# Kernel optimization log

Hardware: AMD Instinct MI355X
Metric: run time of the kernel (lower is better)

The kernel has to match this reference:

```python
import jax, jax.numpy as jnp
import numpy as np
import math

DIM = 512
BLOCK_NUM = 16
SEQ_LEN = 8192
BLOCK_LEN = SEQ_LEN // BLOCK_NUM  # 512 == DIM -> mask used as-is
BATCH = 4
LN_EPS = 1e-3  # keras LayerNormalization default epsilon


def setup_inputs() -> dict:
    key = jax.random.key(0)
    ks = jax.random.split(key, 5)
    inputs = jax.random.normal(ks[0], (BATCH, BLOCK_NUM, BLOCK_LEN, DIM), dtype=jnp.float32)
    # binary padding-style mask, values in {0,1}
    mask_array = jax.random.randint(ks[1], (BATCH, SEQ_LEN, DIM), 0, 2).astype(jnp.float32)
    scale = 1.0 / math.sqrt(DIM)
    dw1 = jax.random.normal(ks[2], (DIM, DIM), dtype=jnp.float32) * scale
    dw2 = jax.random.normal(ks[3], (DIM, DIM), dtype=jnp.float32) * scale
    dw3 = jax.random.normal(ks[4], (DIM, DIM), dtype=jnp.float32) * scale
    db1 = jnp.zeros((DIM,), dtype=jnp.float32)
    db2 = jnp.zeros((DIM,), dtype=jnp.float32)
    db3 = jnp.zeros((DIM,), dtype=jnp.float32)
    return {"inputs": inputs, "mask_array": mask_array,
            "dw1": dw1, "dw2": dw2, "dw3": dw3,
            "db1": db1, "db2": db2, "db3": db3}


def reference(inputs, mask_array, dw1, dw2, dw3, db1, db2, db3):
    # inputs: [B, block_num, block_len, dim]
    Q = jnp.matmul(inputs, dw1) + db1
    K = jnp.matmul(inputs, dw2) + db2
    V = jnpp_matmul = jnp.matmul(inputs, dw3) + db3
    V = jnp.matmul(inputs, dw3) + db3
    # block-local attention scores: [B, bn, bl, bl]
    scores = jnp.einsum('bnqd,bnkd->bnqk', Q, K) / math.sqrt(DIM)
    # mask: [B, seq_len, dim] -> [B, bn, bl, dim]; block_len == dim so no slice/tile
    m = mask_array.reshape(BATCH, BLOCK_NUM, BLOCK_LEN, DIM)
    scores = scores + (1.0 - m) * jnp.float32(-1e10)
    p = jax.nn.softmax(scores, axis=-1)
    out = jnp.einsum('bnqk,bnkd->bnqd', p, V) + inputs  # residual
    # LayerNorm(axis=-1), fresh keras layer: gamma=1, beta=0, eps=1e-3
    mean = jnp.mean(out, axis=-1, keepdims=True)
    var = jnp.mean(jnp.square(out - mean), axis=-1, keepdims=True)
    return (out - mean) / jnp.sqrt(var + LN_EPS)
```

## Files before the change

kernel.cpp:

```cpp
#include <hip/hip_runtime.h>

#define DIMK 512
#define NBLK 64
#define NTOK 32768

typedef short  short8 __attribute__((ext_vector_type(8)));
typedef float  f32x4  __attribute__((ext_vector_type(4)));
typedef unsigned short u16x8 __attribute__((ext_vector_type(8)));

__device__ __forceinline__ unsigned short f2bf(float f) {
  union { float f; unsigned u; } v; v.f = f;
  unsigned r = (v.u + 0x7FFFu + ((v.u >> 16) & 1u)) >> 16;
  return (unsigned short)r;
}
__device__ __forceinline__ float bf2f(unsigned short h) {
  return __uint_as_float(((unsigned)h) << 16);
}

__device__ __forceinline__ void gload_lds16(const unsigned short* g,
                                            unsigned short* l) {
  __builtin_amdgcn_global_load_lds(
      (const __attribute__((address_space(1))) unsigned int*)(g),
      (__attribute__((address_space(3))) unsigned int*)(l),
      16, 0, 0);
}


__global__ __launch_bounds__(256) void k_wt_prep(
    const float* __restrict__ dw1, const float* __restrict__ dw2,
    const float* __restrict__ dw3, unsigned short* __restrict__ Wt)
{
  __shared__ float t[64][65];
  const int b = blockIdx.x;
  const int w = b >> 6;
  const int tt = b & 63;
  const int kt = (tt >> 3) * 64;
  const int nt = (tt & 7) * 64;
  const float* dw = (w == 0) ? dw1 : (w == 1) ? dw2 : dw3;
  const int tid = threadIdx.x;
  const int rr = tid >> 4;
  const int cc = (tid & 15) << 2;

#pragma unroll
  for (int p = 0; p < 4; ++p) {
    const int r = rr + p * 16;
    const float4 v = *(const float4*)&dw[(size_t)(kt + r) * 512 + nt + cc];
    t[cc + 0][r] = v.x; t[cc + 1][r] = v.y;
    t[cc + 2][r] = v.z; t[cc + 3][r] = v.w;
  }
  __syncthreads();
#pragma unroll
  for (int p = 0; p < 4; ++p) {
    const int r = rr + p * 16;
    const int n = nt + r;
    const int k = kt + cc;
    ushort4 o;
    o.x = f2bf(t[r][cc + 0]); o.y = f2bf(t[r][cc + 1]);
    o.z = f2bf(t[r][cc + 2]); o.w = f2bf(t[r][cc + 3]);
    *(ushort4*)&Wt[(size_t)w * 262144 + (size_t)(k >> 5) * 16384 +
                   (size_t)n * 32 + (k & 31)] = o;
  }
}

__global__ __launch_bounds__(256) void k_xconv(
    const float* __restrict__ X, unsigned short* __restrict__ Xb)
{
  const size_t gid = (size_t)blockIdx.x * 256 + threadIdx.x;
  const size_t i = gid * 8;
  const int tok = (int)(i >> 9);
  const int col = (int)(i & 511);
  const float4 a = *(const float4*)(X + i);
  const float4 b = *(const float4*)(X + i + 4);
  u16x8 o;
  o[0] = f2bf(a.x); o[1] = f2bf(a.y); o[2] = f2bf(a.z); o[3] = f2bf(a.w);
  o[4] = f2bf(b.x); o[5] = f2bf(b.y); o[6] = f2bf(b.z); o[7] = f2bf(b.w);
  *(u16x8*)(Xb + ((size_t)(tok >> 7) * 16 + (col >> 5)) * 4096 +
            (tok & 127) * 32 + (col & 31)) = o;
}

__global__ __launch_bounds__(256) void k_bitpack(
    const float* __restrict__ mask, unsigned char* __restrict__ bits)
{
  const size_t gid = (size_t)blockIdx.x * 256 + threadIdx.x;
  const size_t i = gid * 8;
  const float4 ma = *(const float4*)(mask + i);
  const float4 mb = *(const float4*)(mask + i + 4);
  unsigned v = 0;
  v |= (ma.x > 0.5f) << 0; v |= (ma.y > 0.5f) << 1;
  v |= (ma.z > 0.5f) << 2; v |= (ma.w > 0.5f) << 3;
  v |= (mb.x > 0.5f) << 4; v |= (mb.y > 0.5f) << 5;
  v |= (mb.z > 0.5f) << 6; v |= (mb.w > 0.5f) << 7;
  bits[gid] = (unsigned char)v;
}

__global__ __launch_bounds__(256, 2) void k_qkv(
    const unsigned short* __restrict__ Xb, const unsigned short* __restrict__ Wt,
    const float* __restrict__ db1, const float* __restrict__ db2,
    const float* __restrict__ db3,
    unsigned short* __restrict__ Qb, unsigned short* __restrict__ Kb,
    unsigned short* __restrict__ Vt)
{
  __shared__ __align__(16) unsigned short smem[32768];

  const int id = blockIdx.x;
  const int x = id & 7, j = id >> 3;
  const int mtile = x * 32 + (j >> 2);
  const int nt = j & 3;
  const int m0 = mtile * 128;
  const int n0 = nt * 128;

  const int tid = threadIdx.x, lane = tid & 63, wv = tid >> 6;
  const int quad = lane >> 4, l16 = lane & 15;
  const int rb = (wv >> 1) * 64, cb = (wv & 1) * 64;

  f32x4 acc[3][4][4];
#pragma unroll
  for (int w = 0; w < 3; ++w)
#pragma unroll
    for (int i = 0; i < 4; ++i)
#pragma unroll
      for (int jj = 0; jj < 4; ++jj) {
        f32x4 z = {0.f, 0.f, 0.f, 0.f}; acc[w][i][jj] = z;
      }

  auto stage = [&](unsigned short* base, int it) {
    const unsigned short* aslab = Xb + ((size_t)mtile * 16 + it) * 4096;
    gload_lds16(aslab + tid * 8, base + tid * 8);
    gload_lds16(aslab + (tid + 256) * 8, base + (tid + 256) * 8);
#pragma unroll
    for (int h = 0; h < 6; ++h) {
      const int c = tid + h * 256;
      const int w = c >> 9, cc = c & 511;
      const unsigned short* bslab =
          Wt + (size_t)w * 262144 + (size_t)it * 16384 + (size_t)n0 * 32;
      gload_lds16(bslab + cc * 8, base + 4096 + w * 4096 + cc * 8);
    }
  };

  stage(smem, 0);
  __syncthreads();
  int cur = 0;
  for (int it = 0; it < 16; ++it) {
    unsigned short* cbuf = smem + cur * 16384;
    if (it < 15) stage(smem + (cur ^ 1) * 16384, it + 1);
    const unsigned short* As = cbuf;
    const unsigned short* Bs = cbuf + 4096;
    short8 af[4];
#pragma unroll
    for (int i = 0; i < 4; ++i)
      af[i] = *(const short8*)&As[(rb + i * 16 + l16) * 32 + quad * 8];
#pragma unroll
    for (int jj = 0; jj < 4; ++jj)
#pragma unroll
      for (int w = 0; w < 3; ++w) {
        const short8 bf =
            *(const short8*)&Bs[w * 4096 + (cb + jj * 16 + l16) * 32 + quad * 8];
#pragma unroll
        for (int i = 0; i < 4; ++i)
          acc[w][i][jj] = __builtin_amdgcn_mfma_f32_16x16x32_bf16(
              af[i], bf, acc[w][i][jj], 0, 0, 0);
      }
    __syncthreads();
    cur ^= 1;
  }

#pragma unroll
  for (int i = 0; i < 4; ++i)
#pragma unroll
    for (int jj = 0; jj < 4; ++jj)
#pragma unroll
      for (int r = 0; r < 4; ++r) {
        const int tok = m0 + rb + i * 16 + quad * 4 + r;
        const int col = n0 + cb + jj * 16 + l16;
        Qb[((size_t)(tok >> 6) * 16 + (col >> 5)) * 2048 +
           (tok & 63) * 32 + (col & 31)] = f2bf(acc[0][i][jj][r] + db1[col]);
        Kb[((size_t)(tok >> 9) * 16 + (col >> 5)) * 16384 +
           (tok & 511) * 32 + (col & 31)] = f2bf(acc[1][i][jj][r] + db2[col]);
      }
#pragma unroll
  for (int i = 0; i < 4; ++i)
#pragma unroll
    for (int jj = 0; jj < 4; ++jj) {
      const int cl = cb + jj * 16 + l16;
      const int t0 = rb + i * 16 + quad * 4;
      const float bv = db3[n0 + cl];
      ushort4 pk;
      pk.x = f2bf(acc[2][i][jj][0] + bv);
      pk.y = f2bf(acc[2][i][jj][1] + bv);
      pk.z = f2bf(acc[2][i][jj][2] + bv);
      pk.w = f2bf(acc[2][i][jj][3] + bv);
      *(ushort4*)&smem[cl * 136 + t0] = pk;
    }
  __syncthreads();
#pragma unroll
  for (int h = 0; h < 8; ++h) {
    const int c = tid + h * 256;
    const int cl = c >> 4, toff = (c & 15) * 8;
    const int tg = mtile * 128 + toff;
    *(u16x8*)&Vt[(size_t)(tg >> 5) * 16384 + (size_t)(n0 + cl) * 32 +
                 (tg & 31)] = *(const u16x8*)&smem[cl * 136 + toff];
  }
}

__global__ __launch_bounds__(256, 2) void k_attn_p(
    const unsigned short* __restrict__ Qb, const unsigned short* __restrict__ Kb,
    const unsigned long long* __restrict__ bits, unsigned short* __restrict__ Pb)
{
  __shared__ __align__(16) unsigned short smem[36864];
  __shared__ float red[4][64];
  const int tid = threadIdx.x, lane = tid & 63, wv = tid >> 6;
  const int quad = lane >> 4, l16 = lane & 15;
  const int blk = blockIdx.x & 63, mt = blockIdx.x >> 6;
  const size_t q0 = (size_t)blk * 512 + (size_t)mt * 64;
  const int qt = blk * 8 + mt;

  f32x4 acc[4][8];
#pragma unroll
  for (int i = 0; i < 4; ++i)
#pragma unroll
    for (int j = 0; j < 8; ++j) { f32x4 z = {0.f, 0.f, 0.f, 0.f}; acc[i][j] = z; }

  auto stage = [&](unsigned short* base, int it) {
    const unsigned short* aslab = Qb + ((size_t)qt * 16 + it) * 2048;
    gload_lds16(aslab + tid * 8, base + tid * 8);
    const unsigned short* bslab = Kb + ((size_t)blk * 16 + it) * 16384;
#pragma unroll
    for (int h = 0; h < 8; ++h) {
      const int c = tid + h * 256;
      gload_lds16(bslab + c * 8, base + 2048 + c * 8);
    }
  };

  stage(smem, 0);
  __syncthreads();
  int cur = 0;
  for (int it = 0; it < 16; ++it) {
    unsigned short* cbuf = smem + cur * 18432;
    if (it < 15) stage(smem + (cur ^ 1) * 18432, it + 1);
    const unsigned short* As = cbuf;
    const unsigned short* Bs = cbuf + 2048;
    short8 af[4], bfv[8];
#pragma unroll
    for (int i = 0; i < 4; ++i)
      af[i] = *(const short8*)&As[(i * 16 + l16) * 32 + quad * 8];
#pragma unroll
    for (int j = 0; j < 8; ++j)
      bfv[j] = *(const short8*)&Bs[(wv * 128 + j * 16 + l16) * 32 + quad * 8];
#pragma unroll
    for (int i = 0; i < 4; ++i)
#pragma unroll
      for (int j = 0; j < 8; ++j)
        acc[i][j] = __builtin_amdgcn_mfma_f32_16x16x32_bf16(
            af[i], bfv[j], acc[i][j], 0, 0, 0);
    __syncthreads();
    cur ^= 1;
  }

  const float scale = 0.04419417382415922f;
  float rmax[4][4];
#pragma unroll
  for (int i = 0; i < 4; ++i)
#pragma unroll
    for (int r = 0; r < 4; ++r) rmax[i][r] = -3.0e38f;
#pragma unroll
  for (int i = 0; i < 4; ++i)
#pragma unroll
    for (int r = 0; r < 4; ++r) {
      const size_t tok = q0 + i * 16 + quad * 4 + r;
      const unsigned long long w0 = bits[tok * 8 + wv * 2];
      const unsigned long long w1 = bits[tok * 8 + wv * 2 + 1];
#pragma unroll
      for (int j = 0; j < 8; ++j) {
        const unsigned long long sel = (j < 4) ? w0 : w1;
        const float bias = ((sel >> (l16 + 16 * (j & 3))) & 1ull) ? 0.0f : -1e10f;
        const float v = acc[i][j][r] * scale + bias;
        acc[i][j][r] = v;
        rmax[i][r] = fmaxf(rmax[i][r], v);
      }
    }
#pragma unroll
  for (int i = 0; i < 4; ++i)
#pragma unroll
    for (int r = 0; r < 4; ++r)
      for (int d = 1; d < 16; d <<= 1)
        rmax[i][r] = fmaxf(rmax[i][r], __shfl_xor(rmax[i][r], d, 64));
  if (l16 == 0)
#pragma unroll
    for (int i = 0; i < 4; ++i)
#pragma unroll
      for (int r = 0; r < 4; ++r) red[wv][i * 16 + quad * 4 + r] = rmax[i][r];
  __syncthreads();
#pragma unroll
  for (int i = 0; i < 4; ++i)
#pragma unroll
    for (int r = 0; r < 4; ++r) {
      const int row = i * 16 + quad * 4 + r;
      rmax[i][r] = fmaxf(fmaxf(red[0][row], red[1][row]),
                         fmaxf(red[2][row], red[3][row]));
    }
  __syncthreads();
  float rsum[4][4];
#pragma unroll
  for (int i = 0; i < 4; ++i)
#pragma unroll
    for (int r = 0; r < 4; ++r) rsum[i][r] = 0.f;
#pragma unroll
  for (int i = 0; i < 4; ++i)
#pragma unroll
    for (int j = 0; j < 8; ++j)
#pragma unroll
      for (int r = 0; r < 4; ++r) {
        const float e = __expf(acc[i][j][r] - rmax[i][r]);
        acc[i][j][r] = e;
        rsum[i][r] += e;
      }
#pragma unroll
  for (int i = 0; i < 4; ++i)
#pragma unroll
    for (int r = 0; r < 4; ++r)
      for (int d = 1; d < 16; d <<= 1)
        rsum[i][r] += __shfl_xor(rsum[i][r], d, 64);
  if (l16 == 0)
#pragma unroll
    for (int i = 0; i < 4; ++i)
#pragma unroll
      for (int r = 0; r < 4; ++r) red[wv][i * 16 + quad * 4 + r] = rsum[i][r];
  __syncthreads();
#pragma unroll
  for (int i = 0; i < 4; ++i)
#pragma unroll
    for (int r = 0; r < 4; ++r) {
      const int row = i * 16 + quad * 4 + r;
      rsum[i][r] = 1.0f / (red[0][row] + red[1][row] + red[2][row] + red[3][row]);
    }
#pragma unroll
  for (int i = 0; i < 4; ++i)
#pragma unroll
    for (int j = 0; j < 8; ++j)
#pragma unroll
      for (int r = 0; r < 4; ++r) {
        const int tok = (int)(q0 + i * 16 + quad * 4 + r);
        const int col = wv * 128 + j * 16 + l16;
        Pb[((size_t)(tok >> 6) * 16 + (col >> 5)) * 2048 +
           (tok & 63) * 32 + (col & 31)] = f2bf(acc[i][j][r] * rsum[i][r]);
      }
}

__global__ __launch_bounds__(256, 2) void k_pv_ln(
    const unsigned short* __restrict__ Pb, const unsigned short* __restrict__ Vt,
    const unsigned short* __restrict__ Xb, float* __restrict__ Out)
{
  __shared__ __align__(16) unsigned short smem[36864];
  __shared__ float2 red[4][64];
  const int tid = threadIdx.x, lane = tid & 63, wv = tid >> 6;
  const int quad = lane >> 4, l16 = lane & 15;
  const int blk = blockIdx.x & 63, mt = blockIdx.x >> 6;
  const size_t q0 = (size_t)blk * 512 + (size_t)mt * 64;
  const int qt = blk * 8 + mt;

  f32x4 acc[4][8];
#pragma unroll
  for (int i = 0; i < 4; ++i)
#pragma unroll
    for (int j = 0; j < 8; ++j) { f32x4 z = {0.f, 0.f, 0.f, 0.f}; acc[i][j] = z; }

  auto stage = [&](unsigned short* base, int it) {
    const unsigned short* aslab = Pb + ((size_t)qt * 16 + it) * 2048;
    gload_lds16(aslab + tid * 8, base + tid * 8);
    const unsigned short* bslab = Vt + ((size_t)blk * 16 + it) * 16384;
#pragma unroll
    for (int h = 0; h < 8; ++h) {
      const int c = tid + h * 256;
      gload_lds16(bslab + c * 8, base + 2048 + c * 8);
    }
  };

  stage(smem, 0);
  __syncthreads();
  int cur = 0;
  for (int it = 0; it < 16; ++it) {
    unsigned short* cbuf = smem + cur * 18432;
    if (it < 15) stage(smem + (cur ^ 1) * 18432, it + 1);
    const unsigned short* As = cbuf;
    const unsigned short* Bs = cbuf + 2048;
    short8 af[4], bfv[8];
#pragma unroll
    for (int i = 0; i < 4; ++i)
      af[i] = *(const short8*)&As[(i * 16 + l16) * 32 + quad * 8];
#pragma unroll
    for (int j = 0; j < 8; ++j)
      bfv[j] = *(const short8*)&Bs[(wv * 128 + j * 16 + l16) * 32 + quad * 8];
#pragma unroll
    for (int i = 0; i < 4; ++i)
#pragma unroll
      for (int j = 0; j < 8; ++j)
        acc[i][j] = __builtin_amdgcn_mfma_f32_16x16x32_bf16(
            af[i], bfv[j], acc[i][j], 0, 0, 0);
    __syncthreads();
    cur ^= 1;
  }

  float vsum[4][4], vsq[4][4];
#pragma unroll
  for (int i = 0; i < 4; ++i)
#pragma unroll
    for (int r = 0; r < 4; ++r) { vsum[i][r] = 0.f; vsq[i][r] = 0.f; }
#pragma unroll
  for (int i = 0; i < 4; ++i)
#pragma unroll
    for (int j = 0; j < 8; ++j)
#pragma unroll
      for (int r = 0; r < 4; ++r) {
        const int tok = (int)(q0 + i * 16 + quad * 4 + r);
        const int col = wv * 128 + j * 16 + l16;
        const float v = acc[i][j][r] +
            bf2f(Xb[((size_t)(tok >> 7) * 16 + (col >> 5)) * 4096 +
                    (tok & 127) * 32 + (col & 31)]);
        acc[i][j][r] = v;
        vsum[i][r] += v;
        vsq[i][r] += v * v;
      }
#pragma unroll
  for (int i = 0; i < 4; ++i)
#pragma unroll
    for (int r = 0; r < 4; ++r)
      for (int d = 1; d < 16; d <<= 1) {
        vsum[i][r] += __shfl_xor(vsum[i][r], d, 64);
        vsq[i][r]  += __shfl_xor(vsq[i][r], d, 64);
      }
  if (l16 == 0)
#pragma unroll
    for (int i = 0; i < 4; ++i)
#pragma unroll
      for (int r = 0; r < 4; ++r) {
        float2 p; p.x = vsum[i][r]; p.y = vsq[i][r];
        red[wv][i * 16 + quad * 4 + r] = p;
      }
  __syncthreads();
#pragma unroll
  for (int i = 0; i < 4; ++i)
#pragma unroll
    for (int r = 0; r < 4; ++r) {
      const int row = i * 16 + quad * 4 + r;
      float s = 0.f, q = 0.f;
#pragma unroll
      for (int w = 0; w < 4; ++w) { s += red[w][row].x; q += red[w][row].y; }
      const float mean = s * (1.0f / 512.0f);
      const float var  = q * (1.0f / 512.0f) - mean * mean;
      vsum[i][r] = mean;
      vsq[i][r]  = rsqrtf(var + 1e-3f);
    }
#pragma unroll
  for (int i = 0; i < 4; ++i)
#pragma unroll
    for (int j = 0; j < 8; ++j)
#pragma unroll
      for (int r = 0; r < 4; ++r) {
        const size_t tok = q0 + i * 16 + quad * 4 + r;
        const int col = wv * 128 + j * 16 + l16;
        Out[tok * (size_t)DIMK + col] =
            (acc[i][j][r] - vsum[i][r]) * vsq[i][r];
      }
}

extern "C" void kernel_launch(void* const* d_in, const int* in_sizes, int n_in,
                              void* d_out, int out_size, void* d_ws, size_t ws_size,
                              hipStream_t stream)
{
  const float* X    = (const float*)d_in[0];
  const float* mask = (const float*)d_in[1];
  const float* dw1  = (const float*)d_in[2];
  const float* dw2  = (const float*)d_in[3];
  const float* dw3  = (const float*)d_in[4];
  const float* db1  = (const float*)d_in[5];
  const float* db2  = (const float*)d_in[6];
  const float* db3  = (const float*)d_in[7];
  float* Out = (float*)d_out;

  char* ws = (char*)d_ws;
  const size_t MB = 1ull << 20;
  unsigned short* Wt = (unsigned short*)(ws);
  unsigned short* Qb = (unsigned short*)(ws + 2 * MB);
  unsigned short* Kb = (unsigned short*)(ws + 34 * MB);
  unsigned short* Vt = (unsigned short*)(ws + 66 * MB);
  unsigned short* Xb = (unsigned short*)(ws + 98 * MB);
  unsigned short* Pb = Qb;
  unsigned char*  bits = (unsigned char*)d_out;

  k_wt_prep<<<192, 256, 0, stream>>>(dw1, dw2, dw3, Wt);
  k_xconv  <<<8192, 256, 0, stream>>>(X, Xb);
  k_bitpack<<<8192, 256, 0, stream>>>(mask, bits);
  k_qkv    <<<1024, 256, 0, stream>>>(Xb, Wt, db1, db2, db3, Qb, Kb, Vt);
  k_attn_p <<<512, 256, 0, stream>>>(Qb, Kb, (const unsigned long long*)bits, Pb);
  k_pv_ln  <<<512, 256, 0, stream>>>(Pb, Vt, Xb, Out);
}
```

Baseline: 302.8 us.

## Swizzle LDS layout for MFMA operand reads and merge prep kernels into one launch

Applies an XOR swizzle to the 16-byte chunk index when staging tiles into LDS with global_load_lds, so the global source chunk is permuted while the LDS destination stays linear. The MFMA fragment reads use a matching swizzled quad index to reduce LDS bank conflicts in the QKV, QK and PV GEMM loops. It also merges the weight transpose, input bf16 conversion and mask bitpack kernels into a single launch dispatched by block index, cutting two kernel launches. The swizzle must map the same way on both the write and read sides or results will be wrong.

```diff
diff --git a/kernel.cpp b/kernel.cpp
--- a/kernel.cpp
+++ b/kernel.cpp
@@ -25,72 +25,71 @@
       16, 0, 0);
 }
 
-
-__global__ __launch_bounds__(256) void k_wt_prep(
+__device__ __forceinline__ int swz(int c) { return c ^ ((c >> 3) & 3); }
+
+
+__global__ __launch_bounds__(256) void k_prep(
+    const float* __restrict__ X, const float* __restrict__ mask,
     const float* __restrict__ dw1, const float* __restrict__ dw2,
-    const float* __restrict__ dw3, unsigned short* __restrict__ Wt)
+    const float* __restrict__ dw3,
+    unsigned short* __restrict__ Xb, unsigned char* __restrict__ bits,
+    unsigned short* __restrict__ Wt)
 {
   __shared__ float t[64][65];
   const int b = blockIdx.x;
-  const int w = b >> 6;
-  const int tt = b & 63;
-  const int kt = (tt >> 3) * 64;
-  const int nt = (tt & 7) * 64;
-  const float* dw = (w == 0) ? dw1 : (w == 1) ? dw2 : dw3;
   const int tid = threadIdx.x;
-  const int rr = tid >> 4;
-  const int cc = (tid & 15) << 2;
-
-#pragma unroll
-  for (int p = 0; p < 4; ++p) {
-    const int r = rr + p * 16;
-    const float4 v = *(const float4*)&dw[(size_t)(kt + r) * 512 + nt + cc];
-    t[cc + 0][r] = v.x; t[cc + 1][r] = v.y;
-    t[cc + 2][r] = v.z; t[cc + 3][r] = v.w;
+  if (b < 8192) {
+    const size_t gid = (size_t)b * 256 + tid;
+    const size_t i = gid * 8;
+    const int tok = (int)(i >> 9);
+    const int col = (int)(i & 511);
+    const float4 a = *(const float4*)(X + i);
+    const float4 bb = *(const float4*)(X + i + 4);
+    u16x8 o;
+    o[0] = f2bf(a.x); o[1] = f2bf(a.y); o[2] = f2bf(a.z); o[3] = f2bf(a.w);
+    o[4] = f2bf(bb.x); o[5] = f2bf(bb.y); o[6] = f2bf(bb.z); o[7] = f2bf(bb.w);
+    *(u16x8*)(Xb + ((size_t)(tok >> 7) * 16 + (col >> 5)) * 4096 +
+              (tok & 127) * 32 + (col & 31)) = o;
+  } else if (b < 16384) {
+    const size_t gid = (size_t)(b - 8192) * 256 + tid;
+    const size_t i = gid * 8;
+    const float4 ma = *(const float4*)(mask + i);
+    const float4 mb = *(const float4*)(mask + i + 4);
+    unsigned v = 0;
+    v |= (ma.x > 0.5f) << 0; v |= (ma.y > 0.5f) << 1;
+    v |= (ma.z > 0.5f) << 2; v |= (ma.w > 0.5f) << 3;
+    v |= (mb.x > 0.5f) << 4; v |= (mb.y > 0.5f) << 5;
+    v |= (mb.z > 0.5f) << 6; v |= (mb.w > 0.5f) << 7;
+    bits[gid] = (unsigned char)v;
+  } else {
+    const int bb = b - 16384;
+    const int w = bb >> 6;
+    const int tt = bb & 63;
+    const int kt = (tt >> 3) * 64;
+    const int nt = (tt & 7) * 64;
+    const float* dw = (w == 0) ? dw1 : (w == 1) ? dw2 : dw3;
+    const int rr = tid >> 4;
+    const int cc = (tid & 15) << 2;
+#pragma unroll
+    for (int p = 0; p < 4; ++p) {
+      const int r = rr + p * 16;
+      const float4 v = *(const float4*)&dw[(size_t)(kt + r) * 512 + nt + cc];
+      t[cc + 0][r] = v.x; t[cc + 1][r] = v.y;
+      t[cc + 2][r] = v.z; t[cc + 3][r] = v.w;
+    }
+    __syncthreads();
+#pragma unroll
+    for (int p = 0; p < 4; ++p) {
+      const int r = rr + p * 16;
+      const int n = nt + r;
+      const int k = kt + cc;
+      ushort4 o;
+      o.x = f2bf(t[r][cc + 0]); o.y = f2bf(t[r][cc + 1]);
+      o.z = f2bf(t[r][cc + 2]); o.w = f2bf(t[r][cc + 3]);
+      *(ushort4*)&Wt[(size_t)w * 262144 + (size_t)(k >> 5) * 16384 +
+                     (size_t)n * 32 + (k & 31)] = o;
+    }
   }
-  __syncthreads();
-#pragma unroll
-  for (int p = 0; p < 4; ++p) {
-    const int r = rr + p * 16;
-    const int n = nt + r;
-    const int k = kt + cc;
-    ushort4 o;
-    o.x = f2bf(t[r][cc + 0]); o.y = f2bf(t[r][cc + 1]);
-    o.z = f2bf(t[r][cc + 2]); o.w = f2bf(t[r][cc + 3]);
-    *(ushort4*)&Wt[(size_t)w * 262144 + (size_t)(k >> 5) * 16384 +
-                   (size_t)n * 32 + (k & 31)] = o;
-  }
-}
-
-__global__ __launch_bounds__(256) void k_xconv(
-    const float* __restrict__ X, unsigned short* __restrict__ Xb)
-{
-  const size_t gid = (size_t)blockIdx.x * 256 + threadIdx.x;
-  const size_t i = gid * 8;
-  const int tok = (int)(i >> 9);
-  const int col = (int)(i & 511);
-  const float4 a = *(const float4*)(X + i);
-  const float4 b = *(const float4*)(X + i + 4);
-  u16x8 o;
-  o[0] = f2bf(a.x); o[1] = f2bf(a.y); o[2] = f2bf(a.z); o[3] = f2bf(a.w);
-  o[4] = f2bf(b.x); o[5] = f2bf(b.y); o[6] = f2bf(b.z); o[7] = f2bf(b.w);
-  *(u16x8*)(Xb + ((size_t)(tok >> 7) * 16 + (col >> 5)) * 4096 +
-            (tok & 127) * 32 + (col & 31)) = o;
-}
-
-__global__ __launch_bounds__(256) void k_bitpack(
-    const float* __restrict__ mask, unsigned char* __restrict__ bits)
-{
-  const size_t gid = (size_t)blockIdx.x * 256 + threadIdx.x;
-  const size_t i = gid * 8;
-  const float4 ma = *(const float4*)(mask + i);
-  const float4 mb = *(const float4*)(mask + i + 4);
-  unsigned v = 0;
-  v |= (ma.x > 0.5f) << 0; v |= (ma.y > 0.5f) << 1;
-  v |= (ma.z > 0.5f) << 2; v |= (ma.w > 0.5f) << 3;
-  v |= (mb.x > 0.5f) << 4; v |= (mb.y > 0.5f) << 5;
-  v |= (mb.z > 0.5f) << 6; v |= (mb.w > 0.5f) << 7;
-  bits[gid] = (unsigned char)v;
 }
 
 __global__ __launch_bounds__(256, 2) void k_qkv(
@@ -111,6 +110,7 @@
 
   const int tid = threadIdx.x, lane = tid & 63, wv = tid >> 6;
   const int quad = lane >> 4, l16 = lane & 15;
+  const int qx = quad ^ ((l16 >> 1) & 3);
   const int rb = (wv >> 1) * 64, cb = (wv & 1) * 64;
 
   f32x4 acc[3][4][4];
@@ -125,15 +125,15 @@
 
   auto stage = [&](unsigned short* base, int it) {
     const unsigned short* aslab = Xb + ((size_t)mtile * 16 + it) * 4096;
-    gload_lds16(aslab + tid * 8, base + tid * 8);
-    gload_lds16(aslab + (tid + 256) * 8, base + (tid + 256) * 8);
+    gload_lds16(aslab + swz(tid) * 8, base + tid * 8);
+    gload_lds16(aslab + swz(tid + 256) * 8, base + (tid + 256) * 8);
 #pragma unroll
     for (int h = 0; h < 6; ++h) {
       const int c = tid + h * 256;
       const int w = c >> 9, cc = c & 511;
       const unsigned short* bslab =
           Wt + (size_t)w * 262144 + (size_t)it * 16384 + (size_t)n0 * 32;
-      gload_lds16(bslab + cc * 8, base + 4096 + w * 4096 + cc * 8);
+      gload_lds16(bslab + swz(cc) * 8, base + 4096 + w * 4096 + cc * 8);
     }
   };
 
@@ -148,13 +148,13 @@
     short8 af[4];
 #pragma unroll
     for (int i = 0; i < 4; ++i)
-      af[i] = *(const short8*)&As[(rb + i * 16 + l16) * 32 + quad * 8];
+      af[i] = *(const short8*)&As[(rb + i * 16 + l16) * 32 + qx * 8];
 #pragma unroll
     for (int jj = 0; jj < 4; ++jj)
 #pragma unroll
       for (int w = 0; w < 3; ++w) {
         const short8 bf =
-            *(const short8*)&Bs[w * 4096 + (cb + jj * 16 + l16) * 32 + quad * 8];
+            *(const short8*)&Bs[w * 4096 + (cb + jj * 16 + l16) * 32 + qx * 8];
 #pragma unroll
         for (int i = 0; i < 4; ++i)
           acc[w][i][jj] = __builtin_amdgcn_mfma_f32_16x16x32_bf16(
@@ -210,6 +210,7 @@
   __shared__ float red[4][64];
   const int tid = threadIdx.x, lane = tid & 63, wv = tid >> 6;
   const int quad = lane >> 4, l16 = lane & 15;
+  const int qx = quad ^ ((l16 >> 1) & 3);
   const int blk = blockIdx.x & 63, mt = blockIdx.x >> 6;
   const size_t q0 = (size_t)blk * 512 + (size_t)mt * 64;
   const int qt = blk * 8 + mt;
@@ -222,12 +223,12 @@
 
   auto stage = [&](unsigned short* base, int it) {
     const unsigned short* aslab = Qb + ((size_t)qt * 16 + it) * 2048;
-    gload_lds16(aslab + tid * 8, base + tid * 8);
+    gload_lds16(aslab + swz(tid) * 8, base + tid * 8);
     const unsigned short* bslab = Kb + ((size_t)blk * 16 + it) * 16384;
 #pragma unroll
     for (int h = 0; h < 8; ++h) {
       const int c = tid + h * 256;
-      gload_lds16(bslab + c * 8, base + 2048 + c * 8);
+      gload_lds16(bslab + swz(c) * 8, base + 2048 + c * 8);
     }
   };
 
@@ -242,10 +243,10 @@
     short8 af[4], bfv[8];
 #pragma unroll
     for (int i = 0; i < 4; ++i)
-      af[i] = *(const short8*)&As[(i * 16 + l16) * 32 + quad * 8];
-#pragma unroll
-    for (int j = 0; j < 8; ++j)
-      bfv[j] = *(const short8*)&Bs[(wv * 128 + j * 16 + l16) * 32 + quad * 8];
+      af[i] = *(const short8*)&As[(i * 16 + l16) * 32 + qx * 8];
+#pragma unroll
+    for (int j = 0; j < 8; ++j)
+      bfv[j] = *(const short8*)&Bs[(wv * 128 + j * 16 + l16) * 32 + qx * 8];
 #pragma unroll
     for (int i = 0; i < 4; ++i)
 #pragma unroll
@@ -354,6 +355,7 @@
   __shared__ float2 red[4][64];
   const int tid = threadIdx.x, lane = tid & 63, wv = tid >> 6;
   const int quad = lane >> 4, l16 = lane & 15;
+  const int qx = quad ^ ((l16 >> 1) & 3);
   const int blk = blockIdx.x & 63, mt = blockIdx.x >> 6;
   const size_t q0 = (size_t)blk * 512 + (size_t)mt * 64;
   const int qt = blk * 8 + mt;
@@ -366,12 +368,12 @@
 
   auto stage = [&](unsigned short* base, int it) {
     const unsigned short* aslab = Pb + ((size_t)qt * 16 + it) * 2048;
-    gload_lds16(aslab + tid * 8, base + tid * 8);
+    gload_lds16(aslab + swz(tid) * 8, base + tid * 8);
     const unsigned short* bslab = Vt + ((size_t)blk * 16 + it) * 16384;
 #pragma unroll
     for (int h = 0; h < 8; ++h) {
       const int c = tid + h * 256;
-      gload_lds16(bslab + c * 8, base + 2048 + c * 8);
+      gload_lds16(bslab + swz(c) * 8, base + 2048 + c * 8);
     }
   };
 
@@ -386,10 +388,10 @@
     short8 af[4], bfv[8];
 #pragma unroll
     for (int i = 0; i < 4; ++i)
-      af[i] = *(const short8*)&As[(i * 16 + l16) * 32 + quad * 8];
-#pragma unroll
-    for (int j = 0; j < 8; ++j)
-      bfv[j] = *(const short8*)&Bs[(wv * 128 + j * 16 + l16) * 32 + quad * 8];
+      af[i] = *(const short8*)&As[(i * 16 + l16) * 32 + qx * 8];
+#pragma unroll
+    for (int j = 0; j < 8; ++j)
+      bfv[j] = *(const short8*)&Bs[(wv * 128 + j * 16 + l16) * 32 + qx * 8];
 #pragma unroll
     for (int i = 0; i < 4; ++i)
 #pragma unroll
@@ -487,9 +489,7 @@
   unsigned short* Pb = Qb;
   unsigned char*  bits = (unsigned char*)d_out;
 
-  k_wt_prep<<<192, 256, 0, stream>>>(dw1, dw2, dw3, Wt);
-  k_xconv  <<<8192, 256, 0, stream>>>(X, Xb);
-  k_bitpack<<<8192, 256, 0, stream>>>(mask, bits);
+  k_prep   <<<16576, 256, 0, stream>>>(X, mask, dw1, dw2, dw3, Xb, bits, Wt);
   k_qkv    <<<1024, 256, 0, stream>>>(Xb, Wt, db1, db2, db3, Qb, Kb, Vt);
   k_attn_p <<<512, 256, 0, stream>>>(Qb, Kb, (const unsigned long long*)bits, Pb);
   k_pv_ln  <<<512, 256, 0, stream>>>(Pb, Vt, Xb, Out);
```

Result: faster. 295.6 us (-2.4%).
